# Kernel optimization log

Measured on AMD Instinct MI355X. Metric: run time of the kernel, lower is better.

Reference implementation:

```python
import jax, jax.numpy as jnp
import numpy as np

MEM = 32      # mem_size == slot_size (required by role/mem einsum contraction)
SLOT = 32
NREAD = 1
NITER = 3
NIN = 3       # num_input
EPS = 1e-8


def _ln(x, g=None, b=None, eps=1e-5):
    m = x.mean(-1, keepdims=True)
    v = x.var(-1, keepdims=True)
    y = (x - m) / jnp.sqrt(v + eps)
    if g is not None:
        y = y * g + b
    return y


def _lstm_layer(x, Wih, Whh, bih, bhh):
    # x: [S, B, Din]; torch gate order i, f, g, o
    B = x.shape[1]
    H = Whh.shape[1]
    def step(carry, xt):
        h, c = carry
        z = xt @ Wih.T + h @ Whh.T + bih + bhh
        i, f, g, o = jnp.split(z, 4, axis=-1)
        c = jax.nn.sigmoid(f) * c + jax.nn.sigmoid(i) * jnp.tanh(g)
        h = jax.nn.sigmoid(o) * jnp.tanh(c)
        return (h, c), h
    init = (jnp.zeros((B, H), x.dtype), jnp.zeros((B, H), x.dtype))
    _, hs = jax.lax.scan(step, init, x)
    return hs


def _slot_attention(inp, inp_cat, Wi, bi, Wq, bq, Wk, bk, Wv, bv, lng, lnb,
                    Wm1, bm1, Wm2, bm2, Wsp, bsp):
    # inp: [S, B, NIN, 64]; dropout is identity (eval)
    S, B = inp.shape[0], inp.shape[1]
    init_slots = (inp_cat @ Wi.T + bi).reshape(S, B, -1, SLOT)
    k = jax.nn.elu(inp @ Wk.T + bk) + 1.0
    v = inp @ Wv.T + bv
    slots = init_slots
    for _ in range(NITER):
        q = (slots @ Wq.T + bq + init_slots) * SLOT ** (-0.5)
        q = jax.nn.elu(q) + 1.0
        logits = jnp.einsum('sbik,sbjk->sbij', k, q)
        attn = jax.nn.softmax(logits, axis=3) + EPS
        attn = attn / attn.sum(axis=2, keepdims=True)
        upd = jnp.einsum('sbij,sbik->sbjk', attn, v)
        h = _ln(upd, lng, lnb)
        mlp = jax.nn.relu(h @ Wm1.T + bm1) @ Wm2.T + bm2
        slots = slots + mlp / SLOT
    slots = jnp.concatenate([init_slots, slots], axis=-1)
    return slots @ Wsp.T + bsp


def _mask_read(slots, mask, i):
    return jnp.tanh(jnp.einsum('sbne,n->sbe', slots, jnp.roll(mask, i)))


def setup_inputs() -> dict:
    key = jax.random.key(0)
    ks = jax.random.split(key, 20)
    def n(k, shape):
        return jax.random.normal(k, shape, jnp.float32) * 0.05
    z = lambda s: jnp.zeros(s, jnp.float32)
    return {
        'tokens': jax.random.randint(ks[0], (512, 64), 0, 32000),
        'embed_W': n(ks[1], (32000, 256)),
        'Wih0': n(ks[2], (2048, 256)), 'Whh0': n(ks[3], (2048, 512)),
        'bih0': z(2048), 'bhh0': z(2048),
        'Wih1': n(ks[4], (2048, 512)), 'Whh1': n(ks[5], (2048, 512)),
        'bih1': z(2048), 'bhh1': z(2048),
        'Wpi': n(ks[6], (192, 256)), 'bpi': z(192),
        'Wq': n(ks[7], (32, 32)), 'bq': z(32),
        'Wk': n(ks[8], (32, 64)), 'bk': z(32),
        'Wv': n(ks[9], (32, 64)), 'bv': z(32),
        'lng': jnp.ones(32, jnp.float32), 'lnb': z(32),
        'Wm1': n(ks[10], (64, 32)), 'bm1': z(64),
        'Wm2': n(ks[11], (32, 64)), 'bm2': z(32),
        'Wbind': n(ks[12], (96, 192)), 'bbind': z(96),
        'Wreas': n(ks[13], (64, 192)), 'breas': z(64),
        'Wsp': n(ks[14], (32, 64)), 'bsp': z(32),
        'Wg': n(ks[15], (1, 512)), 'bg': z(1),
        'Wout': n(ks[16], (128, 544)), 'bout': z(128),
    }


def reference(tokens, embed_W, Wih0, Whh0, bih0, bhh0, Wih1, Whh1, bih1, bhh1,
              Wpi, bpi, Wq, bq, Wk, bk, Wv, bv, lng, lnb, Wm1, bm1, Wm2, bm2,
              Wbind, bbind, Wreas, breas, Wsp, bsp, Wg, bg, Wout, bout):
    S, B = tokens.shape
    emb = embed_W[tokens]                                   # [S,B,256]
    h = _lstm_layer(emb, Wih0, Whh0, bih0, bhh0)            # [S,B,512]
    h = _lstm_layer(h, Wih1, Whh1, bih1, bhh1)
    dec_in = (emb @ Wpi.T + bpi).reshape(S, B, NIN, -1)     # [S,B,3,64]
    dec_cat = dec_in.reshape(S, B, -1)
    sa = (Wq, bq, Wk, bk, Wv, bv, lng, lnb, Wm1, bm1, Wm2, bm2, Wsp, bsp)
    bind_slots = _slot_attention(dec_in, dec_cat, Wbind, bbind, *sa)  # [S,B,3,32]
    reas_slots = _slot_attention(dec_in, dec_cat, Wreas, breas, *sa)  # [S,B,2,32]
    e = 1e-6
    mask_b = jnp.array([1.0 - 2 * e, e, e], emb.dtype)
    role1 = _mask_read(bind_slots, mask_b, 0)
    role2 = _mask_read(bind_slots, mask_b, 1)
    filler = _mask_read(bind_slots, mask_b, 2)
    mask_r = jnp.array([1.0 - (1 + NREAD) * e, e], emb.dtype)
    u1 = _mask_read(reas_slots, mask_r, 0)
    u2 = _mask_read(reas_slots, mask_r, 1)
    gate = jax.nn.sigmoid(h @ Wg.T + bg + 1.0)              # [S,B,1]

    def step(mem, xs):
        r1, r2, f, g_t, u1t, u2t = xs
        role = jnp.einsum('br,bt->brt', r1, r2)
        prev = jnp.einsum('brt,brtf->bf', role, mem)
        cur = g_t * (f - prev)
        mem = mem + jnp.einsum('brt,bf->brtf', role, cur / MEM)
        nrm = jnp.sqrt(jnp.sum(mem * mem, axis=(1, 2, 3)))
        nrm = jax.nn.relu(nrm - 1.0) + 1.0
        mem = mem / nrm[:, None, None, None]
        read = _ln(jnp.einsum('bsrv,bs,br->bv', mem, u1t, u2t))
        return mem, read

    mem0 = jnp.zeros((B, MEM, MEM, MEM), emb.dtype)
    _, reads = jax.lax.scan(step, mem0, (role1, role2, filler, gate, u1, u2))
    out = jnp.concatenate([h, reads], axis=-1) @ Wout.T + bout
    return out
```

## Files before the change

kernel.cpp:

```cpp
#include <hip/hip_runtime.h>

typedef unsigned short u16;
typedef unsigned int u32;
typedef unsigned long long u64;
typedef __bf16 bf16x8 __attribute__((ext_vector_type(8)));
typedef float f32x4 __attribute__((ext_vector_type(4)));

__device__ __forceinline__ float bf2f(u16 u) { return __uint_as_float(((u32)u) << 16); }
__device__ __forceinline__ u16 f2bf(float f) {
    u32 u = __float_as_uint(f);
    u32 r = (u + 0x7FFFu + ((u >> 16) & 1u)) >> 16;
    return (u16)r;
}
__device__ __forceinline__ float sigm(float x) { return 1.0f / (1.0f + __expf(-x)); }
__device__ __forceinline__ float elu1(float x) { return x > 0.0f ? x + 1.0f : __expf(x); }

__device__ __forceinline__ int ag_load(const int* p) {
    return __hip_atomic_load(p, __ATOMIC_RELAXED, __HIP_MEMORY_SCOPE_AGENT);
}
__device__ __forceinline__ void ag_store(int* p, int v) {
    __hip_atomic_store(p, v, __ATOMIC_RELAXED, __HIP_MEMORY_SCOPE_AGENT);
}
__device__ __forceinline__ void ag_storef(float* p, float v) {
    __hip_atomic_store(p, v, __ATOMIC_RELAXED, __HIP_MEMORY_SCOPE_AGENT);
}
__device__ __forceinline__ void llc_store2(u16* p, u16 a, u16 b) {
    u32 v = (u32)a | ((u32)b << 16);
    __hip_atomic_store((u32*)p, v, __ATOMIC_RELAXED, __HIP_MEMORY_SCOPE_AGENT);
}
__device__ __forceinline__ void llc_store_u16(u16* p, u16 v) {
    __hip_atomic_store(p, v, __ATOMIC_RELAXED, __HIP_MEMORY_SCOPE_AGENT);
}

struct Cvt8 { const float* s[8]; u16* d[8]; int off4[9]; };

__global__ __launch_bounds__(256) void k_f2b8(Cvt8 c)
{
    int i = blockIdx.x * 256 + threadIdx.x;
    if (i >= c.off4[8]) return;
    int k = 0;
#pragma unroll
    for (int q = 1; q < 8; q++) if (i >= c.off4[q]) k = q;
    int j = i - c.off4[k];
    float4 v = ((const float4*)c.s[k])[j];
    ushort4 o;
    o.x = f2bf(v.x); o.y = f2bf(v.y); o.z = f2bf(v.z); o.w = f2bf(v.w);
    ((ushort4*)c.d[k])[j] = o;
}

__global__ __launch_bounds__(256) void k_embed(const int* __restrict__ tok,
                                               const float* __restrict__ W,
                                               u16* __restrict__ out)
{
    int c = blockIdx.x * 256 + threadIdx.x;
    int row = c >> 5, cc = (c & 31) * 8;
    int t = tok[row];
    const float* src = W + (size_t)t * 256 + cc;
    u16 tmp[8];
#pragma unroll
    for (int k = 0; k < 8; k++) tmp[k] = f2bf(src[k]);
    *(uint4*)(out + (size_t)row * 256 + cc) = *(uint4*)tmp;
}

__global__ __launch_bounds__(256) void k_gemm_bt(
    const u16* __restrict__ A, int lda,
    const u16* __restrict__ B,
    u16* __restrict__ Cb, float* __restrict__ Cf, int ldc,
    const float* __restrict__ bias1, const float* __restrict__ bias2,
    int N, int K)
{
    __shared__ u16 As[128][40];
    __shared__ u16 Bs[128][40];
    const int tid = threadIdx.x;
    const int m0 = blockIdx.x * 128, n0 = blockIdx.y * 128;
    const int wave = tid >> 6, lane = tid & 63;
    const int wm = wave & 1, wn = wave >> 1;
    const int quad = lane >> 4, l16 = lane & 15;
    f32x4 acc[4][4] = {};
    for (int k0 = 0; k0 < K; k0 += 32) {
        __syncthreads();
#pragma unroll
        for (int i = 0; i < 2; i++) {
            int c = tid + i * 256, row = c >> 2, cc = (c & 3) * 8;
            *(uint4*)(&As[row][cc]) = *(const uint4*)(A + (size_t)(m0 + row) * lda + k0 + cc);
            uint4 d = {0, 0, 0, 0};
            if (n0 + row < N) d = *(const uint4*)(B + (size_t)(n0 + row) * K + k0 + cc);
            *(uint4*)(&Bs[row][cc]) = d;
        }
        __syncthreads();
        bf16x8 af[4], bfm[4];
#pragma unroll
        for (int x = 0; x < 4; x++) {
            af[x]  = *(const bf16x8*)(&As[wm * 64 + x * 16 + l16][quad * 8]);
            bfm[x] = *(const bf16x8*)(&Bs[wn * 64 + x * 16 + l16][quad * 8]);
        }
#pragma unroll
        for (int mi = 0; mi < 4; mi++)
#pragma unroll
            for (int ni = 0; ni < 4; ni++)
                acc[mi][ni] = __builtin_amdgcn_mfma_f32_16x16x32_bf16(af[mi], bfm[ni], acc[mi][ni], 0, 0, 0);
    }
#pragma unroll
    for (int ni = 0; ni < 4; ni++) {
        int col = n0 + wn * 64 + ni * 16 + l16;
        if (col < N) {
            float bv = 0.f;
            if (bias1) bv += bias1[col];
            if (bias2) bv += bias2[col];
#pragma unroll
            for (int mi = 0; mi < 4; mi++) {
                int r0 = m0 + wm * 64 + mi * 16 + quad * 4;
#pragma unroll
                for (int r = 0; r < 4; r++) {
                    float v = acc[mi][ni][r] + bv;
                    if (Cb) Cb[(size_t)(r0 + r) * ldc + col] = f2bf(v);
                    else    Cf[(size_t)(r0 + r) * ldc + col] = v;
                }
            }
        }
    }
}

struct SmemLstm {
    u16 Wx[32][528];
    u16 Wh[32][528];
    float zs[4][16][33];
};
struct SmemSlot {
    float WqT[32][33], WkT[64][33], WvT[64][33], Wm1T[32][65], Wm2T[64][33], WspT[64][33];
    float bq[32], bk[32], bv[32], bm1[64], bm2[32], bsp[32], g[32], be[32];
    u16 xbuf[8][192];
    float slots[8][3][32], initl[8][3][32], kk[8][3][32], vv[8][3][32], qq[8][3][32];
    float att[8][3][4];
    float ubuf[8][32];
    float hid[8][64];
};
struct SmemScan {
    float r1s[32], r2s[32], fis[32], u1s[32], u2s[32];
    float red[8][32];
    float wred[4];
    float gpart[4];
};
union SmemU {
    SmemLstm l;
    SmemSlot s;
    SmemScan c;
};

__device__ __forceinline__ void stage_slot_weights(SmemSlot& S, const int tid,
    const float* __restrict__ Wq, const float* __restrict__ bq,
    const float* __restrict__ Wk, const float* __restrict__ bk,
    const float* __restrict__ Wv, const float* __restrict__ bv,
    const float* __restrict__ lng, const float* __restrict__ lnb,
    const float* __restrict__ Wm1, const float* __restrict__ bm1,
    const float* __restrict__ Wm2, const float* __restrict__ bm2,
    const float* __restrict__ Wsp, const float* __restrict__ bsp)
{
    for (int i = tid; i < 1024; i += 256) { int o = i >> 5, c = i & 31; S.WqT[c][o] = Wq[o * 32 + c]; }
    for (int i = tid; i < 2048; i += 256) {
        int o6 = i >> 6, c6 = i & 63;
        S.WkT[c6][o6]  = Wk[o6 * 64 + c6];
        S.WvT[c6][o6]  = Wv[o6 * 64 + c6];
        S.Wm2T[c6][o6] = Wm2[o6 * 64 + c6];
        S.WspT[c6][o6] = Wsp[o6 * 64 + c6];
        int o5 = i >> 5, c5 = i & 31;
        S.Wm1T[c5][o5] = Wm1[o5 * 32 + c5];
    }
    if (tid < 32) {
        S.bq[tid] = bq[tid]; S.bk[tid] = bk[tid]; S.bv[tid] = bv[tid];
        S.bm2[tid] = bm2[tid]; S.bsp[tid] = bsp[tid];
        S.g[tid] = lng[tid]; S.be[tid] = lnb[tid];
    }
    if (tid < 64) S.bm1[tid] = bm1[tid];
}

template <int NSLOT>
__device__ __forceinline__ void slot_unit(
    SmemSlot& S, const int tid, const size_t row0,
    const u16* __restrict__ dec, const u16* __restrict__ initp,
    float* __restrict__ o1, float* __restrict__ o2, float* __restrict__ o3)
{
    const int p = tid >> 5, l = tid & 31;
    const size_t row = row0 + p;
    for (int i = l; i < 192; i += 32) S.xbuf[p][i] = dec[row * 192 + i];
    __syncthreads();
#pragma unroll
    for (int i = 0; i < 3; i++) {
        float aK = S.bk[l], aV = S.bv[l];
        for (int c = 0; c < 64; c++) {
            float x = bf2f(S.xbuf[p][i * 64 + c]);
            aK += x * S.WkT[c][l];
            aV += x * S.WvT[c][l];
        }
        S.kk[p][i][l] = elu1(aK);
        S.vv[p][i][l] = aV;
    }
#pragma unroll
    for (int j = 0; j < NSLOT; j++) {
        float iv = bf2f(initp[row * (NSLOT * 32) + j * 32 + l]);
        S.initl[p][j][l] = iv;
        S.slots[p][j][l] = iv;
    }
    __syncthreads();
    const float rs = 0.17677669529663687f;
    for (int it = 0; it < 3; it++) {
#pragma unroll
        for (int j = 0; j < NSLOT; j++) {
            float a = S.bq[l];
            for (int c = 0; c < 32; c++) a += S.slots[p][j][c] * S.WqT[c][l];
            S.qq[p][j][l] = elu1((a + S.initl[p][j][l]) * rs);
        }
        __syncthreads();
        if (l < 3 * NSLOT) {
            int i = l / NSLOT, j = l % NSLOT;
            float s = 0.f;
            for (int c = 0; c < 32; c++) s += S.kk[p][i][c] * S.qq[p][j][c];
            S.att[p][i][j] = s;
        }
        __syncthreads();
        if (l < 3) {
            float mx = -1e30f;
            for (int j = 0; j < NSLOT; j++) mx = fmaxf(mx, S.att[p][l][j]);
            float sm = 0.f, ex[3];
            for (int j = 0; j < NSLOT; j++) { ex[j] = __expf(S.att[p][l][j] - mx); sm += ex[j]; }
            for (int j = 0; j < NSLOT; j++) S.att[p][l][j] = ex[j] / sm + 1e-8f;
        }
        __syncthreads();
        if (l < NSLOT) {
            float s = S.att[p][0][l] + S.att[p][1][l] + S.att[p][2][l];
            float inv = 1.0f / s;
            for (int i = 0; i < 3; i++) S.att[p][i][l] *= inv;
        }
        __syncthreads();
#pragma unroll
        for (int j = 0; j < NSLOT; j++) {
            float u = S.att[p][0][j] * S.vv[p][0][l] + S.att[p][1][j] * S.vv[p][1][l] + S.att[p][2][j] * S.vv[p][2][l];
            float mean = u;
            for (int mk = 1; mk < 32; mk <<= 1) mean += __shfl_xor(mean, mk, 32);
            mean *= (1.0f / 32.0f);
            float d = u - mean;
            float var = d * d;
            for (int mk = 1; mk < 32; mk <<= 1) var += __shfl_xor(var, mk, 32);
            var *= (1.0f / 32.0f);
            float y = d * rsqrtf(var + 1e-5f) * S.g[l] + S.be[l];
            S.ubuf[p][l] = y;
            __syncthreads();
#pragma unroll
            for (int oo = 0; oo < 2; oo++) {
                int o = l + oo * 32;
                float a = S.bm1[o];
                for (int c = 0; c < 32; c++) a += S.ubuf[p][c] * S.Wm1T[c][o];
                S.hid[p][o] = fmaxf(a, 0.f);
            }
            __syncthreads();
            float a2 = S.bm2[l];
            for (int c = 0; c < 64; c++) a2 += S.hid[p][c] * S.Wm2T[c][l];
            S.slots[p][j][l] += a2 * (1.0f / 32.0f);
            __syncthreads();
        }
    }
    float pj[NSLOT];
#pragma unroll
    for (int j = 0; j < NSLOT; j++) {
        float a = S.bsp[l];
        for (int c = 0; c < 32; c++) a += S.initl[p][j][c] * S.WspT[c][l];
        for (int c = 0; c < 32; c++) a += S.slots[p][j][c] * S.WspT[32 + c][l];
        pj[j] = a;
    }
    const float e = 1e-6f, me = (float)(1.0 - 2e-6);
    if (NSLOT == 3) {
        ag_storef(&o1[row * 32 + l], tanhf(me * pj[0] + e * pj[1] + e * pj[2]));
        ag_storef(&o2[row * 32 + l], tanhf(e * pj[0] + me * pj[1] + e * pj[2]));
        ag_storef(&o3[row * 32 + l], tanhf(e * pj[0] + e * pj[1] + me * pj[2]));
    } else {
        ag_storef(&o1[row * 32 + l], tanhf(me * pj[0] + e * pj[1]));
        ag_storef(&o2[row * 32 + l], tanhf(e * pj[0] + me * pj[1]));
    }
}

__global__ __launch_bounds__(256) void k_mega(
    const u16* __restrict__ emb,
    const u16* __restrict__ Wx0, const u16* __restrict__ Wh0,
    const u16* __restrict__ Wx1, const u16* __restrict__ Wh1,
    const float* __restrict__ bi0, const float* __restrict__ bh0,
    const float* __restrict__ bi1, const float* __restrict__ bh1,
    u16* __restrict__ h0seq,
    u16* __restrict__ h1seq,
    u16* __restrict__ acat,
    int* __restrict__ flags,
    float* __restrict__ r1, float* __restrict__ r2,
    float* __restrict__ fi, float* __restrict__ uu1, float* __restrict__ uu2,
    const float* __restrict__ Wg, const float* __restrict__ bg,
    const u16* __restrict__ dec,
    const u16* __restrict__ initb, const u16* __restrict__ initr,
    const float* __restrict__ Wq, const float* __restrict__ bq,
    const float* __restrict__ Wk, const float* __restrict__ bk,
    const float* __restrict__ Wv, const float* __restrict__ bv,
    const float* __restrict__ lng, const float* __restrict__ lnb,
    const float* __restrict__ Wm1, const float* __restrict__ bm1,
    const float* __restrict__ Wm2, const float* __restrict__ bm2,
    const float* __restrict__ Wsp, const float* __restrict__ bsp)
{
    __shared__ SmemU sm;
    const int tid = threadIdx.x;
    const int blk = blockIdx.x;
    int* f0   = flags;
    int* f1   = flags + 4096;
    int* f1s  = flags + 8192;
    int* prog = flags + 12288;

    if (blk < 128) {
        auto& Wx = sm.l.Wx;
        auto& Wh = sm.l.Wh;
        auto& zs = sm.l.zs;
        const int layer = blk >> 6;
        const int me = blk & 63;
        const int jbase = me * 8;
        const int Kx = layer ? 512 : 256;
        const u16* Wxp = layer ? Wx1 : Wx0;
        const u16* Whp = layer ? Wh1 : Wh0;
        const float* bi = layer ? bi1 : bi0;
        const float* bh = layer ? bh1 : bh0;
#pragma unroll
        for (int i = 0; i < 8; i++) {
            int c = tid + i * 256;
            int row = c >> 6, cc = (c & 63) * 8;
            int grow = (row >> 3) * 512 + jbase + (row & 7);
            *(uint4*)(&Wh[row][cc]) = *(const uint4*)(Whp + (size_t)grow * 512 + cc);
        }
        {
            int cpr = Kx >> 3;
            int iters = (32 * cpr) >> 8;
            for (int i = 0; i < iters; i++) {
                int c = tid + i * 256;
                int row = c / cpr, cc = (c % cpr) * 8;
                int grow = (row >> 3) * 512 + jbase + (row & 7);
                *(uint4*)(&Wx[row][cc]) = *(const uint4*)(Wxp + (size_t)grow * Kx + cc);
            }
        }
        const int wave = tid >> 6, lane = tid & 63;
        const int quad = lane >> 4, l16 = lane & 15;
        const int m = wave * 16 + l16;
        const int bl = lane >> 2;
        const int b = wave * 16 + bl;
        const int jj = (lane & 3) * 2;
        const int hoff = quad * 512 + m * 8;
        float bia0[4], bia1[4];
#pragma unroll
        for (int g = 0; g < 4; g++) {
            bia0[g] = bi[g * 512 + jbase + jj]     + bh[g * 512 + jbase + jj];
            bia1[g] = bi[g * 512 + jbase + jj + 1] + bh[g * 512 + jbase + jj + 1];
        }
        const int pollOwn = (wave * 64 + lane) * 16;
        const int pubIdx  = (wave * 64 + me) * 16;
        float c0 = 0.f, c1 = 0.f;
        __syncthreads();
        for (int t = 0; t < 512; t++) {
            f32x4 acc0 = {}, acc1 = {};
            if (!layer) {
                const u16* xrow = emb + ((size_t)t * 64 + m) * 256;
#pragma unroll
                for (int kc = 0; kc < 8; kc++) {
                    bf16x8 a  = *(const bf16x8*)(xrow + kc * 32 + quad * 8);
                    bf16x8 w0 = *(const bf16x8*)(&Wx[l16][kc * 32 + quad * 8]);
                    bf16x8 w1 = *(const bf16x8*)(&Wx[16 + l16][kc * 32 + quad * 8]);
                    acc0 = __builtin_amdgcn_mfma_f32_16x16x32_bf16(a, w0, acc0, 0, 0, 0);
                    acc1 = __builtin_amdgcn_mfma_f32_16x16x32_bf16(a, w1, acc1, 0, 0, 0);
                }
                if (t > 0) {
                    int it = 0;
                    for (;;) {
                        int a = ag_load(f0 + pollOwn);
                        if (__all(a >= t)) break;
                        if (++it > 3000000) break;
                        __builtin_amdgcn_s_sleep(1);
                    }
                    const u16* hrd = h0seq + (size_t)(t - 1) * 32768 + hoff;
#pragma unroll
                    for (int kc = 0; kc < 16; kc++) {
                        bf16x8 a  = *(const bf16x8*)(hrd + kc * 2048);
                        bf16x8 w0 = *(const bf16x8*)(&Wh[l16][kc * 32 + quad * 8]);
                        bf16x8 w1 = *(const bf16x8*)(&Wh[16 + l16][kc * 32 + quad * 8]);
                        acc0 = __builtin_amdgcn_mfma_f32_16x16x32_bf16(a, w0, acc0, 0, 0, 0);
                        acc1 = __builtin_amdgcn_mfma_f32_16x16x32_bf16(a, w1, acc1, 0, 0, 0);
                    }
                }
            } else {
                {
                    int it = 0;
                    for (;;) {
                        int a = ag_load(f0 + pollOwn);
                        if (__all(a >= t + 1)) break;
                        if (++it > 3000000) break;
                        __builtin_amdgcn_s_sleep(1);
                    }
                }
                const u16* xrow = h0seq + (size_t)t * 32768 + hoff;
#pragma unroll
                for (int kc = 0; kc < 16; kc++) {
                    bf16x8 a  = *(const bf16x8*)(xrow + kc * 2048);
                    bf16x8 w0 = *(const bf16x8*)(&Wx[l16][kc * 32 + quad * 8]);
                    bf16x8 w1 = *(const bf16x8*)(&Wx[16 + l16][kc * 32 + quad * 8]);
                    acc0 = __builtin_amdgcn_mfma_f32_16x16x32_bf16(a, w0, acc0, 0, 0, 0);
                    acc1 = __builtin_amdgcn_mfma_f32_16x16x32_bf16(a, w1, acc1, 0, 0, 0);
                }
                if (t > 0) {
                    int it = 0;
                    for (;;) {
                        int a = ag_load(f1 + pollOwn);
                        if (__all(a >= t)) break;
                        if (++it > 3000000) break;
                        __builtin_amdgcn_s_sleep(1);
                    }
                    const u16* hrd = h1seq + (size_t)(t - 1) * 32768 + hoff;
#pragma unroll
                    for (int kc = 0; kc < 16; kc++) {
                        bf16x8 a  = *(const bf16x8*)(hrd + kc * 2048);
                        bf16x8 w0 = *(const bf16x8*)(&Wh[l16][kc * 32 + quad * 8]);
                        bf16x8 w1 = *(const bf16x8*)(&Wh[16 + l16][kc * 32 + quad * 8]);
                        acc0 = __builtin_amdgcn_mfma_f32_16x16x32_bf16(a, w0, acc0, 0, 0, 0);
                        acc1 = __builtin_amdgcn_mfma_f32_16x16x32_bf16(a, w1, acc1, 0, 0, 0);
                    }
                }
            }
#pragma unroll
            for (int r = 0; r < 4; r++) {
                zs[wave][quad * 4 + r][l16]      = acc0[r];
                zs[wave][quad * 4 + r][16 + l16] = acc1[r];
            }
            u16 hb0, hb1;
            {
                float zi0 = zs[wave][bl][jj]      + bia0[0];
                float zf0 = zs[wave][bl][8 + jj]  + bia0[1];
                float zg0 = zs[wave][bl][16 + jj] + bia0[2];
                float zo0 = zs[wave][bl][24 + jj] + bia0[3];
                c0 = sigm(zf0) * c0 + sigm(zi0) * tanhf(zg0);
                float h0v = sigm(zo0) * tanhf(c0);
                float zi1 = zs[wave][bl][jj + 1]      + bia1[0];
                float zf1 = zs[wave][bl][8 + jj + 1]  + bia1[1];
                float zg1 = zs[wave][bl][16 + jj + 1] + bia1[2];
                float zo1 = zs[wave][bl][24 + jj + 1] + bia1[3];
                c1 = sigm(zf1) * c1 + sigm(zi1) * tanhf(zg1);
                float h1v = sigm(zo1) * tanhf(c1);
                hb0 = f2bf(h0v); hb1 = f2bf(h1v);
            }
            if (!layer) {
                llc_store2(h0seq + (size_t)t * 32768 + me * 512 + b * 8 + jj, hb0, hb1);
                __builtin_amdgcn_s_waitcnt(0);
                if (lane == 0) ag_store(f0 + pubIdx, t + 1);
            } else {
                llc_store2(h1seq + (size_t)t * 32768 + me * 512 + b * 8 + jj, hb0, hb1);
                __builtin_amdgcn_s_waitcnt(0);
                if (lane == 0) ag_store(f1 + pubIdx, t + 1);
                llc_store2(acat + ((size_t)t * 64 + b) * 544 + jbase + jj, hb0, hb1);
                __builtin_amdgcn_s_waitcnt(0);
                if (lane == 0) ag_store(f1s + pubIdx, t + 1);
            }
        }
    } else if (blk < 192) {
        const int sb = blk - 128;
        const int grp = sb >> 4;
        const int f = tid & 31, rg = tid >> 5;
        float m[4][32];
#pragma unroll
        for (int x = 0; x < 4; x++)
            for (int y = 0; y < 32; y++) m[x][y] = 0.f;
        auto& r1s = sm.c.r1s;
        auto& r2s = sm.c.r2s;
        auto& fis = sm.c.fis;
        auto& u1s = sm.c.u1s;
        auto& u2s = sm.c.u2s;
        auto& red = sm.c.red;
        auto& wred = sm.c.wred;
        auto& gpart = sm.c.gpart;
        float wg0 = Wg[2 * tid], wg1 = Wg[2 * tid + 1];
        float bgv = bg[0];
        for (int t = 0; t < 512; t++) {
            if (tid < 64) {
                int* p1 = f1s + (grp * 64 + tid) * 16;
                int it = 0;
                for (;;) {
                    int a = ag_load(p1);
                    if (__all(a >= t + 1)) break;
                    if (++it > 3000000) break;
                    __builtin_amdgcn_s_sleep(1);
                }
            } else if (tid < 128) {
                const int k = tid - 64;
                const int* pp = prog + k * 16;
                const int need = (t + 1) * 16;
                int it = 0;
                for (;;) {
                    int a = 0x7FFFFFFF;
                    if (k < 63) a = ag_load(pp);
                    if (__all(a >= need)) break;
                    if (++it > 3000000) break;
                    __builtin_amdgcn_s_sleep(1);
                }
            }
            __syncthreads();
            float pre = 0.f;
            {
                size_t base = ((size_t)t * 64 + sb) * 32;
                if (tid < 32) pre = r1[base + tid];
                else if (tid < 64) pre = r2[base + tid - 32];
                else if (tid < 96) pre = fi[base + tid - 64];
                else if (tid < 128) pre = uu1[base + tid - 96];
                else if (tid < 160) pre = uu2[base + tid - 128];
            }
            {
                const u16* hr = acat + ((size_t)t * 64 + sb) * 544;
                u32 hv = *(const u32*)(hr + 2 * tid);
                float gp = bf2f((u16)hv) * wg0 + bf2f((u16)(hv >> 16)) * wg1;
                for (int mk = 1; mk < 64; mk <<= 1) gp += __shfl_xor(gp, mk, 64);
                if ((tid & 63) == 0) gpart[tid >> 6] = gp;
            }
            if (tid < 32) r1s[tid] = pre;
            else if (tid < 64) r2s[tid - 32] = pre;
            else if (tid < 96) fis[tid - 64] = pre;
            else if (tid < 128) u1s[tid - 96] = pre;
            else if (tid < 160) u2s[tid - 128] = pre;
            __syncthreads();
            float gsh = sigm(gpart[0] + gpart[1] + gpart[2] + gpart[3] + bgv + 1.0f);
            float p = 0.f;
#pragma unroll
            for (int rl = 0; rl < 4; rl++) {
                float s = 0.f;
                for (int ti = 0; ti < 32; ti++) s += r2s[ti] * m[rl][ti];
                p += r1s[rg * 4 + rl] * s;
            }
            red[rg][f] = p;
            __syncthreads();
            float prev = 0.f;
#pragma unroll
            for (int g = 0; g < 8; g++) prev += red[g][f];
            float curo = gsh * (fis[f] - prev) * (1.0f / 32.0f);
            float nsq = 0.f;
#pragma unroll
            for (int rl = 0; rl < 4; rl++) {
                float a = r1s[rg * 4 + rl] * curo;
                for (int ti = 0; ti < 32; ti++) {
                    m[rl][ti] += a * r2s[ti];
                    nsq += m[rl][ti] * m[rl][ti];
                }
            }
            for (int mk = 1; mk < 64; mk <<= 1) nsq += __shfl_xor(nsq, mk, 64);
            __syncthreads();
            if ((tid & 63) == 0) wred[tid >> 6] = nsq;
            __syncthreads();
            float nrm = sqrtf(wred[0] + wred[1] + wred[2] + wred[3]);
            float sc = nrm > 1.0f ? 1.0f / nrm : 1.0f;
            float rp = 0.f;
#pragma unroll
            for (int rl = 0; rl < 4; rl++) {
                float s = 0.f;
                for (int ti = 0; ti < 32; ti++) {
                    m[rl][ti] *= sc;
                    s += m[rl][ti] * u2s[ti];
                }
                rp += u1s[rg * 4 + rl] * s;
            }
            red[rg][f] = rp;
            __syncthreads();
            float rv = 0.f;
#pragma unroll
            for (int g = 0; g < 8; g++) rv += red[g][f];
            float mean = rv;
            for (int mk = 1; mk < 32; mk <<= 1) mean += __shfl_xor(mean, mk, 32);
            mean *= (1.0f / 32.0f);
            float d = rv - mean;
            float var = d * d;
            for (int mk = 1; mk < 32; mk <<= 1) var += __shfl_xor(var, mk, 32);
            var *= (1.0f / 32.0f);
            if (tid < 32) {
                float y = d * rsqrtf(var + 1e-5f);
                llc_store_u16(acat + ((size_t)t * 64 + sb) * 544 + 512 + f, f2bf(y));
            }
            __syncthreads();
        }
    } else {
        const int wid = blk - 192;
        stage_slot_weights(sm.s, tid, Wq, bq, Wk, bk, Wv, bv, lng, lnb,
                           Wm1, bm1, Wm2, bm2, Wsp, bsp);
        __syncthreads();
        int* myprog = prog + wid * 16;
        for (int u = wid; u < 8192; u += 63) {
            const int t = u >> 4, s = u & 15;
            if (s < 8)
                slot_unit<3>(sm.s, tid, (size_t)t * 64 + s * 8, dec, initb, r1, r2, fi);
            else
                slot_unit<2>(sm.s, tid, (size_t)t * 64 + (s - 8) * 8, dec, initr, uu1, uu2, nullptr);
            __builtin_amdgcn_s_waitcnt(0);
            __syncthreads();
            if (tid == 0) ag_store(myprog, u + 63);
        }
    }
}

extern "C" void kernel_launch(void* const* d_in, const int* in_sizes, int n_in,
                              void* d_out, int out_size, void* d_ws, size_t ws_size,
                              hipStream_t stream)
{
    (void)in_sizes; (void)n_in; (void)out_size; (void)ws_size;
    const int*   tokens = (const int*)d_in[0];
    const float* embW  = (const float*)d_in[1];
    const float* Wih0  = (const float*)d_in[2];
    const float* Whh0  = (const float*)d_in[3];
    const float* bih0  = (const float*)d_in[4];
    const float* bhh0  = (const float*)d_in[5];
    const float* Wih1  = (const float*)d_in[6];
    const float* Whh1  = (const float*)d_in[7];
    const float* bih1  = (const float*)d_in[8];
    const float* bhh1  = (const float*)d_in[9];
    const float* Wpi   = (const float*)d_in[10];
    const float* bpi   = (const float*)d_in[11];
    const float* Wq    = (const float*)d_in[12];
    const float* bq    = (const float*)d_in[13];
    const float* Wk    = (const float*)d_in[14];
    const float* bk    = (const float*)d_in[15];
    const float* Wv    = (const float*)d_in[16];
    const float* bv    = (const float*)d_in[17];
    const float* lng   = (const float*)d_in[18];
    const float* lnb   = (const float*)d_in[19];
    const float* Wm1   = (const float*)d_in[20];
    const float* bm1   = (const float*)d_in[21];
    const float* Wm2   = (const float*)d_in[22];
    const float* bm2   = (const float*)d_in[23];
    const float* Wbind = (const float*)d_in[24];
    const float* bbind = (const float*)d_in[25];
    const float* Wreas = (const float*)d_in[26];
    const float* breas = (const float*)d_in[27];
    const float* Wsp   = (const float*)d_in[28];
    const float* bsp   = (const float*)d_in[29];
    const float* Wg    = (const float*)d_in[30];
    const float* bg    = (const float*)d_in[31];
    const float* Wout  = (const float*)d_in[32];
    const float* bout  = (const float*)d_in[33];

    char* ws = (char*)d_ws;
    size_t off = 0;
    auto alloc = [&](size_t bytes) { size_t o = off; off += (bytes + 255) & ~(size_t)255; return o; };
    int*  flags  = (int*)(ws + alloc(16384 * 4));
    u16*  emb    = (u16*)(ws + alloc(32768ull * 256 * 2));
    u16*  dec    = (u16*)(ws + alloc(32768ull * 192 * 2));
    u16*  initb  = (u16*)(ws + alloc(32768ull * 96 * 2));
    u16*  initr  = (u16*)(ws + alloc(32768ull * 64 * 2));
    u16*  acat   = (u16*)(ws + alloc(32768ull * 544 * 2));
    u16*  h0seq  = (u16*)(ws + alloc(512ull * 64 * 512 * 2));
    u16*  h1seq  = (u16*)(ws + alloc(512ull * 64 * 512 * 2));
    float* role1 = (float*)(ws + alloc(32768ull * 32 * 4));
    float* role2 = (float*)(ws + alloc(32768ull * 32 * 4));
    float* fill  = (float*)(ws + alloc(32768ull * 32 * 4));
    float* u1v   = (float*)(ws + alloc(32768ull * 32 * 4));
    float* u2v   = (float*)(ws + alloc(32768ull * 32 * 4));
    u16* Wx0b  = (u16*)(ws + alloc(2048ull * 256 * 2));
    u16* Wh0b  = (u16*)(ws + alloc(2048ull * 512 * 2));
    u16* Wx1b  = (u16*)(ws + alloc(2048ull * 512 * 2));
    u16* Wh1b  = (u16*)(ws + alloc(2048ull * 512 * 2));
    u16* Wpib  = (u16*)(ws + alloc(192ull * 256 * 2));
    u16* Wbindb = (u16*)(ws + alloc(96ull * 192 * 2));
    u16* Wreasb = (u16*)(ws + alloc(64ull * 192 * 2));
    u16* Woutb  = (u16*)(ws + alloc(128ull * 544 * 2));

    hipMemsetAsync(flags, 0, 16384 * 4, stream);
    {
        Cvt8 c;
        const float* s[8] = {Wih0, Whh0, Wih1, Whh1, Wpi, Wbind, Wreas, Wout};
        u16* d[8] = {Wx0b, Wh0b, Wx1b, Wh1b, Wpib, Wbindb, Wreasb, Woutb};
        int n[8] = {2048 * 256, 2048 * 512, 2048 * 512, 2048 * 512,
                    192 * 256, 96 * 192, 64 * 192, 128 * 544};
        int acc = 0;
        for (int k = 0; k < 8; k++) { c.s[k] = s[k]; c.d[k] = d[k]; c.off4[k] = acc; acc += n[k] / 4; }
        c.off4[8] = acc;
        k_f2b8<<<(acc + 255) / 256, 256, 0, stream>>>(c);
    }
    k_embed<<<4096, 256, 0, stream>>>(tokens, embW, emb);
    k_gemm_bt<<<dim3(256, 2), 256, 0, stream>>>(emb, 256, Wpib, dec, nullptr, 192, bpi, nullptr, 192, 256);
    k_gemm_bt<<<dim3(256, 1), 256, 0, stream>>>(dec, 192, Wbindb, initb, nullptr, 96, bbind, nullptr, 96, 192);
    k_gemm_bt<<<dim3(256, 1), 256, 0, stream>>>(dec, 192, Wreasb, initr, nullptr, 64, breas, nullptr, 64, 192);
    k_mega<<<255, 256, 0, stream>>>(emb, Wx0b, Wh0b, Wx1b, Wh1b,
                                    bih0, bhh0, bih1, bhh1,
                                    h0seq, h1seq, acat, flags,
                                    role1, role2, fill, u1v, u2v, Wg, bg,
                                    dec, initb, initr,
                                    Wq, bq, Wk, bk, Wv, bv, lng, lnb,
                                    Wm1, bm1, Wm2, bm2, Wsp, bsp);
    k_gemm_bt<<<dim3(256, 1), 256, 0, stream>>>(acat, 544, Woutb, nullptr, (float*)d_out, 128, bout, nullptr, 128, 544);
}
```

Baseline: 3.276 ms.

## Split slot-attention work out of persistent megakernel into a separate pre-pass kernel

Measured after the change: 3.645 ms. 11.3% more time.

```diff
diff --git a/kernel.cpp b/kernel.cpp
--- a/kernel.cpp
+++ b/kernel.cpp
@@ -19,9 +19,6 @@
     return __hip_atomic_load(p, __ATOMIC_RELAXED, __HIP_MEMORY_SCOPE_AGENT);
 }
 __device__ __forceinline__ void ag_store(int* p, int v) {
-    __hip_atomic_store(p, v, __ATOMIC_RELAXED, __HIP_MEMORY_SCOPE_AGENT);
-}
-__device__ __forceinline__ void ag_storef(float* p, float v) {
     __hip_atomic_store(p, v, __ATOMIC_RELAXED, __HIP_MEMORY_SCOPE_AGENT);
 }
 __device__ __forceinline__ void llc_store2(u16* p, u16 a, u16 b) {
@@ -121,11 +118,6 @@
     }
 }
 
-struct SmemLstm {
-    u16 Wx[32][528];
-    u16 Wh[32][528];
-    float zs[4][16][33];
-};
 struct SmemSlot {
     float WqT[32][33], WkT[64][33], WvT[64][33], Wm1T[32][65], Wm2T[64][33], WspT[64][33];
     float bq[32], bk[32], bv[32], bm1[64], bm2[32], bsp[32], g[32], be[32];
@@ -134,17 +126,6 @@
     float att[8][3][4];
     float ubuf[8][32];
     float hid[8][64];
-};
-struct SmemScan {
-    float r1s[32], r2s[32], fis[32], u1s[32], u2s[32];
-    float red[8][32];
-    float wred[4];
-    float gpart[4];
-};
-union SmemU {
-    SmemLstm l;
-    SmemSlot s;
-    SmemScan c;
 };
 
 __device__ __forceinline__ void stage_slot_weights(SmemSlot& S, const int tid,
@@ -269,12 +250,40 @@
     }
     const float e = 1e-6f, me = (float)(1.0 - 2e-6);
     if (NSLOT == 3) {
-        ag_storef(&o1[row * 32 + l], tanhf(me * pj[0] + e * pj[1] + e * pj[2]));
-        ag_storef(&o2[row * 32 + l], tanhf(e * pj[0] + me * pj[1] + e * pj[2]));
-        ag_storef(&o3[row * 32 + l], tanhf(e * pj[0] + e * pj[1] + me * pj[2]));
+        o1[row * 32 + l] = tanhf(me * pj[0] + e * pj[1] + e * pj[2]);
+        o2[row * 32 + l] = tanhf(e * pj[0] + me * pj[1] + e * pj[2]);
+        o3[row * 32 + l] = tanhf(e * pj[0] + e * pj[1] + me * pj[2]);
     } else {
-        ag_storef(&o1[row * 32 + l], tanhf(me * pj[0] + e * pj[1]));
-        ag_storef(&o2[row * 32 + l], tanhf(e * pj[0] + me * pj[1]));
+        o1[row * 32 + l] = tanhf(me * pj[0] + e * pj[1]);
+        o2[row * 32 + l] = tanhf(e * pj[0] + me * pj[1]);
+    }
+}
+
+__global__ __launch_bounds__(256) void k_slotsweep(
+    const u16* __restrict__ dec,
+    const u16* __restrict__ initb, const u16* __restrict__ initr,
+    const float* __restrict__ Wq, const float* __restrict__ bq,
+    const float* __restrict__ Wk, const float* __restrict__ bk,
+    const float* __restrict__ Wv, const float* __restrict__ bv,
+    const float* __restrict__ lng, const float* __restrict__ lnb,
+    const float* __restrict__ Wm1, const float* __restrict__ bm1,
+    const float* __restrict__ Wm2, const float* __restrict__ bm2,
+    const float* __restrict__ Wsp, const float* __restrict__ bsp,
+    float* __restrict__ r1, float* __restrict__ r2, float* __restrict__ fi,
+    float* __restrict__ u1, float* __restrict__ u2)
+{
+    __shared__ SmemSlot S;
+    const int tid = threadIdx.x;
+    stage_slot_weights(S, tid, Wq, bq, Wk, bk, Wv, bv, lng, lnb,
+                       Wm1, bm1, Wm2, bm2, Wsp, bsp);
+    __syncthreads();
+    for (int u = blockIdx.x; u < 8192; u += 256) {
+        const int t = u >> 4, s = u & 15;
+        if (s < 8)
+            slot_unit<3>(S, tid, (size_t)t * 64 + s * 8, dec, initb, r1, r2, fi);
+        else
+            slot_unit<2>(S, tid, (size_t)t * 64 + (s - 8) * 8, dec, initr, u1, u2, nullptr);
+        __syncthreads();
     }
 }
 
@@ -288,31 +297,21 @@
     u16* __restrict__ h1seq,
     u16* __restrict__ acat,
     int* __restrict__ flags,
-    float* __restrict__ r1, float* __restrict__ r2,
-    float* __restrict__ fi, float* __restrict__ uu1, float* __restrict__ uu2,
-    const float* __restrict__ Wg, const float* __restrict__ bg,
-    const u16* __restrict__ dec,
-    const u16* __restrict__ initb, const u16* __restrict__ initr,
-    const float* __restrict__ Wq, const float* __restrict__ bq,
-    const float* __restrict__ Wk, const float* __restrict__ bk,
-    const float* __restrict__ Wv, const float* __restrict__ bv,
-    const float* __restrict__ lng, const float* __restrict__ lnb,
-    const float* __restrict__ Wm1, const float* __restrict__ bm1,
-    const float* __restrict__ Wm2, const float* __restrict__ bm2,
-    const float* __restrict__ Wsp, const float* __restrict__ bsp)
-{
-    __shared__ SmemU sm;
+    const float* __restrict__ r1, const float* __restrict__ r2,
+    const float* __restrict__ fi, const float* __restrict__ uu1,
+    const float* __restrict__ uu2,
+    const float* __restrict__ Wg, const float* __restrict__ bg)
+{
     const int tid = threadIdx.x;
     const int blk = blockIdx.x;
-    int* f0   = flags;
-    int* f1   = flags + 4096;
-    int* f1s  = flags + 8192;
-    int* prog = flags + 12288;
+    int* f0  = flags;
+    int* f1  = flags + 4096;
+    int* f1s = flags + 8192;
 
     if (blk < 128) {
-        auto& Wx = sm.l.Wx;
-        auto& Wh = sm.l.Wh;
-        auto& zs = sm.l.zs;
+        __shared__ u16 Wx[32][528];
+        __shared__ u16 Wh[32][528];
+        __shared__ float zs[4][16][33];
         const int layer = blk >> 6;
         const int me = blk & 63;
         const int jbase = me * 8;
@@ -457,7 +456,7 @@
                 if (lane == 0) ag_store(f1s + pubIdx, t + 1);
             }
         }
-    } else if (blk < 192) {
+    } else {
         const int sb = blk - 128;
         const int grp = sb >> 4;
         const int f = tid & 31, rg = tid >> 5;
@@ -465,17 +464,22 @@
 #pragma unroll
         for (int x = 0; x < 4; x++)
             for (int y = 0; y < 32; y++) m[x][y] = 0.f;
-        auto& r1s = sm.c.r1s;
-        auto& r2s = sm.c.r2s;
-        auto& fis = sm.c.fis;
-        auto& u1s = sm.c.u1s;
-        auto& u2s = sm.c.u2s;
-        auto& red = sm.c.red;
-        auto& wred = sm.c.wred;
-        auto& gpart = sm.c.gpart;
+        __shared__ float r1s[32], r2s[32], fis[32], u1s[32], u2s[32];
+        __shared__ float red[8][32];
+        __shared__ float wred[4];
+        __shared__ float gpart[4];
         float wg0 = Wg[2 * tid], wg1 = Wg[2 * tid + 1];
         float bgv = bg[0];
         for (int t = 0; t < 512; t++) {
+            float pre = 0.f;
+            {
+                size_t base = ((size_t)t * 64 + sb) * 32;
+                if (tid < 32) pre = r1[base + tid];
+                else if (tid < 64) pre = r2[base + tid - 32];
+                else if (tid < 96) pre = fi[base + tid - 64];
+                else if (tid < 128) pre = uu1[base + tid - 96];
+                else if (tid < 160) pre = uu2[base + tid - 128];
+            }
             if (tid < 64) {
                 int* p1 = f1s + (grp * 64 + tid) * 16;
                 int it = 0;
@@ -485,29 +489,13 @@
                     if (++it > 3000000) break;
                     __builtin_amdgcn_s_sleep(1);
                 }
-            } else if (tid < 128) {
-                const int k = tid - 64;
-                const int* pp = prog + k * 16;
-                const int need = (t + 1) * 16;
-                int it = 0;
-                for (;;) {
-                    int a = 0x7FFFFFFF;
-                    if (k < 63) a = ag_load(pp);
-                    if (__all(a >= need)) break;
-                    if (++it > 3000000) break;
-                    __builtin_amdgcn_s_sleep(1);
-                }
-            }
-            __syncthreads();
-            float pre = 0.f;
-            {
-                size_t base = ((size_t)t * 64 + sb) * 32;
-                if (tid < 32) pre = r1[base + tid];
-                else if (tid < 64) pre = r2[base + tid - 32];
-                else if (tid < 96) pre = fi[base + tid - 64];
-                else if (tid < 128) pre = uu1[base + tid - 96];
-                else if (tid < 160) pre = uu2[base + tid - 128];
-            }
+            }
+            __syncthreads();
+            if (tid < 32) r1s[tid] = pre;
+            else if (tid < 64) r2s[tid - 32] = pre;
+            else if (tid < 96) fis[tid - 64] = pre;
+            else if (tid < 128) u1s[tid - 96] = pre;
+            else if (tid < 160) u2s[tid - 128] = pre;
             {
                 const u16* hr = acat + ((size_t)t * 64 + sb) * 544;
                 u32 hv = *(const u32*)(hr + 2 * tid);
@@ -515,11 +503,6 @@
                 for (int mk = 1; mk < 64; mk <<= 1) gp += __shfl_xor(gp, mk, 64);
                 if ((tid & 63) == 0) gpart[tid >> 6] = gp;
             }
-            if (tid < 32) r1s[tid] = pre;
-            else if (tid < 64) r2s[tid - 32] = pre;
-            else if (tid < 96) fis[tid - 64] = pre;
-            else if (tid < 128) u1s[tid - 96] = pre;
-            else if (tid < 160) u2s[tid - 128] = pre;
             __syncthreads();
             float gsh = sigm(gpart[0] + gpart[1] + gpart[2] + gpart[3] + bgv + 1.0f);
             float p = 0.f;
@@ -577,22 +560,6 @@
                 llc_store_u16(acat + ((size_t)t * 64 + sb) * 544 + 512 + f, f2bf(y));
             }
             __syncthreads();
-        }
-    } else {
-        const int wid = blk - 192;
-        stage_slot_weights(sm.s, tid, Wq, bq, Wk, bk, Wv, bv, lng, lnb,
-                           Wm1, bm1, Wm2, bm2, Wsp, bsp);
-        __syncthreads();
-        int* myprog = prog + wid * 16;
-        for (int u = wid; u < 8192; u += 63) {
-            const int t = u >> 4, s = u & 15;
-            if (s < 8)
-                slot_unit<3>(sm.s, tid, (size_t)t * 64 + s * 8, dec, initb, r1, r2, fi);
-            else
-                slot_unit<2>(sm.s, tid, (size_t)t * 64 + (s - 8) * 8, dec, initr, uu1, uu2, nullptr);
-            __builtin_amdgcn_s_waitcnt(0);
-            __syncthreads();
-            if (tid == 0) ag_store(myprog, u + 63);
         }
     }
 }
@@ -678,12 +645,13 @@
     k_gemm_bt<<<dim3(256, 2), 256, 0, stream>>>(emb, 256, Wpib, dec, nullptr, 192, bpi, nullptr, 192, 256);
     k_gemm_bt<<<dim3(256, 1), 256, 0, stream>>>(dec, 192, Wbindb, initb, nullptr, 96, bbind, nullptr, 96, 192);
     k_gemm_bt<<<dim3(256, 1), 256, 0, stream>>>(dec, 192, Wreasb, initr, nullptr, 64, breas, nullptr, 64, 192);
-    k_mega<<<255, 256, 0, stream>>>(emb, Wx0b, Wh0b, Wx1b, Wh1b,
+    k_slotsweep<<<256, 256, 0, stream>>>(dec, initb, initr,
+                                         Wq, bq, Wk, bk, Wv, bv, lng, lnb,
+                                         Wm1, bm1, Wm2, bm2, Wsp, bsp,
+                                         role1, role2, fill, u1v, u2v);
+    k_mega<<<192, 256, 0, stream>>>(emb, Wx0b, Wh0b, Wx1b, Wh1b,
                                     bih0, bhh0, bih1, bhh1,
                                     h0seq, h1seq, acat, flags,
-                                    role1, role2, fill, u1v, u2v, Wg, bg,
-                                    dec, initb, initr,
-                                    Wq, bq, Wk, bk, Wv, bv, lng, lnb,
-                                    Wm1, bm1, Wm2, bm2, Wsp, bsp);
+                                    role1, role2, fill, u1v, u2v, Wg, bg);
     k_gemm_bt<<<dim3(256, 1), 256, 0, stream>>>(acat, 544, Woutb, nullptr, (float*)d_out, 128, bout, nullptr, 128, 544);
 }
```

## Keep slot-attention weights in registers, use wave barriers, add a slot worker block

Applied to the files above, without the earlier changes.

After: 5.010 ms. +52.9%, slower.

```diff
diff --git a/kernel.cpp b/kernel.cpp
--- a/kernel.cpp
+++ b/kernel.cpp
@@ -14,6 +14,8 @@
 }
 __device__ __forceinline__ float sigm(float x) { return 1.0f / (1.0f + __expf(-x)); }
 __device__ __forceinline__ float elu1(float x) { return x > 0.0f ? x + 1.0f : __expf(x); }
+
+__device__ __forceinline__ void wb() { __builtin_amdgcn_wave_barrier(); }
 
 __device__ __forceinline__ int ag_load(const int* p) {
     return __hip_atomic_load(p, __ATOMIC_RELAXED, __HIP_MEMORY_SCOPE_AGENT);
@@ -127,7 +129,7 @@
     float zs[4][16][33];
 };
 struct SmemSlot {
-    float WqT[32][33], WkT[64][33], WvT[64][33], Wm1T[32][65], Wm2T[64][33], WspT[64][33];
+    float WqT[32][33], Wm1T[32][65], WspT[64][33];
     float bq[32], bk[32], bv[32], bm1[64], bm2[32], bsp[32], g[32], be[32];
     u16 xbuf[8][192];
     float slots[8][3][32], initl[8][3][32], kk[8][3][32], vv[8][3][32], qq[8][3][32];
@@ -149,19 +151,15 @@
 
 __device__ __forceinline__ void stage_slot_weights(SmemSlot& S, const int tid,
     const float* __restrict__ Wq, const float* __restrict__ bq,
-    const float* __restrict__ Wk, const float* __restrict__ bk,
-    const float* __restrict__ Wv, const float* __restrict__ bv,
+    const float* __restrict__ bk, const float* __restrict__ bv,
     const float* __restrict__ lng, const float* __restrict__ lnb,
     const float* __restrict__ Wm1, const float* __restrict__ bm1,
-    const float* __restrict__ Wm2, const float* __restrict__ bm2,
+    const float* __restrict__ bm2,
     const float* __restrict__ Wsp, const float* __restrict__ bsp)
 {
     for (int i = tid; i < 1024; i += 256) { int o = i >> 5, c = i & 31; S.WqT[c][o] = Wq[o * 32 + c]; }
     for (int i = tid; i < 2048; i += 256) {
         int o6 = i >> 6, c6 = i & 63;
-        S.WkT[c6][o6]  = Wk[o6 * 64 + c6];
-        S.WvT[c6][o6]  = Wv[o6 * 64 + c6];
-        S.Wm2T[c6][o6] = Wm2[o6 * 64 + c6];
         S.WspT[c6][o6] = Wsp[o6 * 64 + c6];
         int o5 = i >> 5, c5 = i & 31;
         S.Wm1T[c5][o5] = Wm1[o5 * 32 + c5];
@@ -178,22 +176,31 @@
 __device__ __forceinline__ void slot_unit(
     SmemSlot& S, const int tid, const size_t row0,
     const u16* __restrict__ dec, const u16* __restrict__ initp,
+    const float* __restrict__ wk, const float* __restrict__ wv,
+    const float* __restrict__ wm2,
     float* __restrict__ o1, float* __restrict__ o2, float* __restrict__ o3)
 {
     const int p = tid >> 5, l = tid & 31;
     const size_t row = row0 + p;
     for (int i = l; i < 192; i += 32) S.xbuf[p][i] = dec[row * 192 + i];
-    __syncthreads();
+    wb();
 #pragma unroll
     for (int i = 0; i < 3; i++) {
-        float aK = S.bk[l], aV = S.bv[l];
-        for (int c = 0; c < 64; c++) {
-            float x = bf2f(S.xbuf[p][i * 64 + c]);
-            aK += x * S.WkT[c][l];
-            aV += x * S.WvT[c][l];
-        }
-        S.kk[p][i][l] = elu1(aK);
-        S.vv[p][i][l] = aV;
+        float k0 = 0.f, k1 = 0.f, v0 = 0.f, v1 = 0.f;
+#pragma unroll
+        for (int c = 0; c < 64; c += 4) {
+            u64 xw = *(const u64*)(&S.xbuf[p][i * 64 + c]);
+            float x0 = bf2f((u16)xw);
+            float x1 = bf2f((u16)(xw >> 16));
+            float x2 = bf2f((u16)(xw >> 32));
+            float x3 = bf2f((u16)(xw >> 48));
+            k0 += x0 * wk[c];     k1 += x1 * wk[c + 1];
+            k0 += x2 * wk[c + 2]; k1 += x3 * wk[c + 3];
+            v0 += x0 * wv[c];     v1 += x1 * wv[c + 1];
+            v0 += x2 * wv[c + 2]; v1 += x3 * wv[c + 3];
+        }
+        S.kk[p][i][l] = elu1(S.bk[l] + (k0 + k1));
+        S.vv[p][i][l] = S.bv[l] + (v0 + v1);
     }
 #pragma unroll
     for (int j = 0; j < NSLOT; j++) {
@@ -201,23 +208,34 @@
         S.initl[p][j][l] = iv;
         S.slots[p][j][l] = iv;
     }
-    __syncthreads();
+    wb();
     const float rs = 0.17677669529663687f;
     for (int it = 0; it < 3; it++) {
 #pragma unroll
         for (int j = 0; j < NSLOT; j++) {
-            float a = S.bq[l];
-            for (int c = 0; c < 32; c++) a += S.slots[p][j][c] * S.WqT[c][l];
-            S.qq[p][j][l] = elu1((a + S.initl[p][j][l]) * rs);
-        }
-        __syncthreads();
+            float a0 = 0.f, a1 = 0.f, a2 = 0.f, a3 = 0.f;
+#pragma unroll
+            for (int c = 0; c < 32; c += 4) {
+                f32x4 sv = *(const f32x4*)(&S.slots[p][j][c]);
+                a0 += sv[0] * S.WqT[c][l];     a1 += sv[1] * S.WqT[c + 1][l];
+                a2 += sv[2] * S.WqT[c + 2][l]; a3 += sv[3] * S.WqT[c + 3][l];
+            }
+            S.qq[p][j][l] = elu1((S.bq[l] + ((a0 + a1) + (a2 + a3)) + S.initl[p][j][l]) * rs);
+        }
+        wb();
         if (l < 3 * NSLOT) {
             int i = l / NSLOT, j = l % NSLOT;
-            float s = 0.f;
-            for (int c = 0; c < 32; c++) s += S.kk[p][i][c] * S.qq[p][j][c];
-            S.att[p][i][j] = s;
-        }
-        __syncthreads();
+            float a0 = 0.f, a1 = 0.f, a2 = 0.f, a3 = 0.f;
+#pragma unroll
+            for (int c = 0; c < 32; c += 4) {
+                f32x4 kv = *(const f32x4*)(&S.kk[p][i][c]);
+                f32x4 qv = *(const f32x4*)(&S.qq[p][j][c]);
+                a0 += kv[0] * qv[0]; a1 += kv[1] * qv[1];
+                a2 += kv[2] * qv[2]; a3 += kv[3] * qv[3];
+            }
+            S.att[p][i][j] = (a0 + a1) + (a2 + a3);
+        }
+        wb();
         if (l < 3) {
             float mx = -1e30f;
             for (int j = 0; j < NSLOT; j++) mx = fmaxf(mx, S.att[p][l][j]);
@@ -225,13 +243,13 @@
             for (int j = 0; j < NSLOT; j++) { ex[j] = __expf(S.att[p][l][j] - mx); sm += ex[j]; }
             for (int j = 0; j < NSLOT; j++) S.att[p][l][j] = ex[j] / sm + 1e-8f;
         }
-        __syncthreads();
+        wb();
         if (l < NSLOT) {
             float s = S.att[p][0][l] + S.att[p][1][l] + S.att[p][2][l];
             float inv = 1.0f / s;
             for (int i = 0; i < 3; i++) S.att[p][i][l] *= inv;
         }
-        __syncthreads();
+        wb();
 #pragma unroll
         for (int j = 0; j < NSLOT; j++) {
             float u = S.att[p][0][j] * S.vv[p][0][l] + S.att[p][1][j] * S.vv[p][1][l] + S.att[p][2][j] * S.vv[p][2][l];
@@ -244,28 +262,48 @@
             var *= (1.0f / 32.0f);
             float y = d * rsqrtf(var + 1e-5f) * S.g[l] + S.be[l];
             S.ubuf[p][l] = y;
-            __syncthreads();
+            wb();
 #pragma unroll
             for (int oo = 0; oo < 2; oo++) {
                 int o = l + oo * 32;
-                float a = S.bm1[o];
-                for (int c = 0; c < 32; c++) a += S.ubuf[p][c] * S.Wm1T[c][o];
-                S.hid[p][o] = fmaxf(a, 0.f);
-            }
-            __syncthreads();
-            float a2 = S.bm2[l];
-            for (int c = 0; c < 64; c++) a2 += S.hid[p][c] * S.Wm2T[c][l];
-            S.slots[p][j][l] += a2 * (1.0f / 32.0f);
-            __syncthreads();
+                float a0 = 0.f, a1 = 0.f, a2 = 0.f, a3 = 0.f;
+#pragma unroll
+                for (int c = 0; c < 32; c += 4) {
+                    f32x4 uv = *(const f32x4*)(&S.ubuf[p][c]);
+                    a0 += uv[0] * S.Wm1T[c][o];     a1 += uv[1] * S.Wm1T[c + 1][o];
+                    a2 += uv[2] * S.Wm1T[c + 2][o]; a3 += uv[3] * S.Wm1T[c + 3][o];
+                }
+                S.hid[p][o] = fmaxf(S.bm1[o] + ((a0 + a1) + (a2 + a3)), 0.f);
+            }
+            wb();
+            float a0 = 0.f, a1 = 0.f, a2 = 0.f, a3 = 0.f;
+#pragma unroll
+            for (int c = 0; c < 64; c += 4) {
+                f32x4 hv = *(const f32x4*)(&S.hid[p][c]);
+                a0 += hv[0] * wm2[c];     a1 += hv[1] * wm2[c + 1];
+                a2 += hv[2] * wm2[c + 2]; a3 += hv[3] * wm2[c + 3];
+            }
+            S.slots[p][j][l] += (S.bm2[l] + ((a0 + a1) + (a2 + a3))) * (1.0f / 32.0f);
+            wb();
         }
     }
     float pj[NSLOT];
 #pragma unroll
     for (int j = 0; j < NSLOT; j++) {
-        float a = S.bsp[l];
-        for (int c = 0; c < 32; c++) a += S.initl[p][j][c] * S.WspT[c][l];
-        for (int c = 0; c < 32; c++) a += S.slots[p][j][c] * S.WspT[32 + c][l];
-        pj[j] = a;
+        float a0 = 0.f, a1 = 0.f, a2 = 0.f, a3 = 0.f;
+#pragma unroll
+        for (int c = 0; c < 32; c += 4) {
+            f32x4 iv = *(const f32x4*)(&S.initl[p][j][c]);
+            a0 += iv[0] * S.WspT[c][l];     a1 += iv[1] * S.WspT[c + 1][l];
+            a2 += iv[2] * S.WspT[c + 2][l]; a3 += iv[3] * S.WspT[c + 3][l];
+        }
+#pragma unroll
+        for (int c = 0; c < 32; c += 4) {
+            f32x4 sv = *(const f32x4*)(&S.slots[p][j][c]);
+            a0 += sv[0] * S.WspT[32 + c][l];     a1 += sv[1] * S.WspT[32 + c + 1][l];
+            a2 += sv[2] * S.WspT[32 + c + 2][l]; a3 += sv[3] * S.WspT[32 + c + 3][l];
+        }
+        pj[j] = S.bsp[l] + ((a0 + a1) + (a2 + a3));
     }
     const float e = 1e-6f, me = (float)(1.0 - 2e-6);
     if (NSLOT == 3) {
@@ -491,8 +529,7 @@
                 const int need = (t + 1) * 16;
                 int it = 0;
                 for (;;) {
-                    int a = 0x7FFFFFFF;
-                    if (k < 63) a = ag_load(pp);
+                    int a = ag_load(pp);
                     if (__all(a >= need)) break;
                     if (++it > 3000000) break;
                     __builtin_amdgcn_s_sleep(1);
@@ -580,19 +617,29 @@
         }
     } else {
         const int wid = blk - 192;
-        stage_slot_weights(sm.s, tid, Wq, bq, Wk, bk, Wv, bv, lng, lnb,
-                           Wm1, bm1, Wm2, bm2, Wsp, bsp);
+        stage_slot_weights(sm.s, tid, Wq, bq, bk, bv, lng, lnb,
+                           Wm1, bm1, bm2, Wsp, bsp);
+        const int l = tid & 31;
+        float wk[64], wv[64], wm2c[64];
+#pragma unroll
+        for (int c = 0; c < 64; c += 4) {
+            *(float4*)&wk[c]   = *(const float4*)(Wk  + l * 64 + c);
+            *(float4*)&wv[c]   = *(const float4*)(Wv  + l * 64 + c);
+            *(float4*)&wm2c[c] = *(const float4*)(Wm2 + l * 64 + c);
+        }
         __syncthreads();
         int* myprog = prog + wid * 16;
-        for (int u = wid; u < 8192; u += 63) {
+        for (int u = wid; u < 8192; u += 64) {
             const int t = u >> 4, s = u & 15;
             if (s < 8)
-                slot_unit<3>(sm.s, tid, (size_t)t * 64 + s * 8, dec, initb, r1, r2, fi);
+                slot_unit<3>(sm.s, tid, (size_t)t * 64 + s * 8, dec, initb,
+                             wk, wv, wm2c, r1, r2, fi);
             else
-                slot_unit<2>(sm.s, tid, (size_t)t * 64 + (s - 8) * 8, dec, initr, uu1, uu2, nullptr);
+                slot_unit<2>(sm.s, tid, (size_t)t * 64 + (s - 8) * 8, dec, initr,
+                             wk, wv, wm2c, uu1, uu2, nullptr);
             __builtin_amdgcn_s_waitcnt(0);
             __syncthreads();
-            if (tid == 0) ag_store(myprog, u + 63);
+            if (tid == 0) ag_store(myprog, u + 64);
         }
     }
 }
@@ -678,7 +725,7 @@
     k_gemm_bt<<<dim3(256, 2), 256, 0, stream>>>(emb, 256, Wpib, dec, nullptr, 192, bpi, nullptr, 192, 256);
     k_gemm_bt<<<dim3(256, 1), 256, 0, stream>>>(dec, 192, Wbindb, initb, nullptr, 96, bbind, nullptr, 96, 192);
     k_gemm_bt<<<dim3(256, 1), 256, 0, stream>>>(dec, 192, Wreasb, initr, nullptr, 64, breas, nullptr, 64, 192);
-    k_mega<<<255, 256, 0, stream>>>(emb, Wx0b, Wh0b, Wx1b, Wh1b,
+    k_mega<<<256, 256, 0, stream>>>(emb, Wx0b, Wh0b, Wx1b, Wh1b,
                                     bih0, bhh0, bih1, bhh1,
                                     h0seq, h1seq, acat, flags,
                                     role1, role2, fill, u1v, u2v, Wg, bg,
```
